# Kernel optimization log

Hardware: AMD Instinct MI355X
Metric: run time of the kernel (lower is better)

Reference implementation:

```python
import jax, jax.numpy as jnp
import numpy as np

GEOM_W = 0.01
N_ITERS = 3
HUBER_DELTA = 0.5
LM_EPS = 1e-6

def _skew(w):
    x, y, z = w[..., 0], w[..., 1], w[..., 2]
    o = jnp.zeros_like(x)
    return jnp.stack([jnp.stack([o, -z, y], -1),
                      jnp.stack([z, o, -x], -1),
                      jnp.stack([-y, x, o], -1)], -2)

def _se3_exp(xi):
    # xi = [omega(3), v(3)]; returns [B,4,4] left-multiplicative increment
    w, v = xi[:, :3], xi[:, 3:]
    th2 = jnp.sum(w * w, -1)
    small = th2 < 1e-8
    th2s = jnp.where(small, 1.0, th2)
    th = jnp.sqrt(th2s)
    A = jnp.where(small, 1.0 - th2 / 6.0, jnp.sin(th) / th)
    Bc = jnp.where(small, 0.5 - th2 / 24.0, (1.0 - jnp.cos(th)) / th2s)
    Cc = jnp.where(small, 1.0 / 6.0 - th2 / 120.0, (th - jnp.sin(th)) / (th2s * th))
    K = _skew(w)
    K2 = jnp.einsum('bij,bjk->bik', K, K)
    I3 = jnp.eye(3, dtype=xi.dtype)
    R = I3 + A[:, None, None] * K + Bc[:, None, None] * K2
    V = I3 + Bc[:, None, None] * K + Cc[:, None, None] * K2
    t = jnp.einsum('bij,bj->bi', V, v)
    T = jnp.zeros((xi.shape[0], 4, 4), xi.dtype)
    return T.at[:, :3, :3].set(R).at[:, :3, 3].set(t).at[:, 3, 3].set(1.0)

def _xy_grid(H, W, K):
    fx, fy, cx, cy = [K[:, i][:, None, None, None] for i in range(4)]
    uu = jnp.arange(W, dtype=K.dtype)[None, None, None, :]
    vv = jnp.arange(H, dtype=K.dtype)[None, None, :, None]
    return (uu - cx) / fx, (vv - cy) / fy  # [B,1,1,W], [B,1,H,1]

def _compute_vertex(d, px, py):
    return jnp.concatenate([px * d, py * d, d], 1)  # [B,3,H,W]

def _central_diff(F):
    fp = jnp.pad(F, ((0, 0), (0, 0), (0, 0), (1, 1)), mode='edge')
    dx = (fp[:, :, :, 2:] - fp[:, :, :, :-2]) * 0.5
    fp = jnp.pad(F, ((0, 0), (0, 0), (1, 1), (0, 0)), mode='edge')
    dy = (fp[:, :, 2:, :] - fp[:, :, :-2, :]) * 0.5
    return dx, dy

def _compute_normal(V):
    dvdx, dvdy = _central_diff(V)
    n = jnp.cross(jnp.moveaxis(dvdx, 1, -1), jnp.moveaxis(dvdy, 1, -1))
    n = jnp.moveaxis(n, -1, 1)
    return n / jnp.sqrt(jnp.sum(n * n, 1, keepdims=True) + 1e-12)

def _bilinear(F, u, v):
    # F [B,C,H,W]; u,v [B,N] pixel coords; zero padding bilinear -> [B,C,N]
    B, C, H, W = F.shape
    N = u.shape[1]
    u0, v0 = jnp.floor(u), jnp.floor(v)
    du, dv = u - u0, v - v0
    Ff = F.reshape(B, C, H * W)
    def gat(ui, vi, w):
        inb = (ui >= 0) & (ui <= W - 1) & (vi >= 0) & (vi <= H - 1)
        uc = jnp.clip(ui, 0, W - 1).astype(jnp.int32)
        vc = jnp.clip(vi, 0, H - 1).astype(jnp.int32)
        idx = jnp.broadcast_to((vc * W + uc)[:, None, :], (B, C, N))
        return jnp.take_along_axis(Ff, idx, axis=2) * (w * inb.astype(F.dtype))[:, None, :]
    return (gat(u0, v0, (1 - du) * (1 - dv)) + gat(u0 + 1, v0, du * (1 - dv)) +
            gat(u0, v0 + 1, (1 - du) * dv) + gat(u0 + 1, v0 + 1, du * dv))

def _grid_sample(F, grid):
    # grid [B,H,W,2] in [-1,1], align_corners=True, zero padding
    B, C, H, W = F.shape
    u = (grid[..., 0] + 1.0) * 0.5 * (W - 1)
    v = (grid[..., 1] + 1.0) * 0.5 * (H - 1)
    return _bilinear(F, u.reshape(B, -1), v.reshape(B, -1)).reshape(B, C, H, W)

def _icp_sigma(dpt, normal_r, R):
    sxy, sdisp, baseline, focal = 5.5, 0.4, 1.2, 525.0
    B, _, H, W = normal_r.shape
    sd = jnp.concatenate([dpt / focal * sxy, dpt / focal * sxy,
                          dpt * dpt * sdisp / (focal * baseline)], 1)
    J = jnp.einsum('bcn,bci->bin', normal_r.reshape(B, 3, H * W), R).reshape(B, 3, H, W)
    cov = jnp.sum(J * sd * sd * J, 1, keepdims=True)
    return jnp.sqrt(cov + 1e-8)

def _icp(V0, V1, N0, N1, T, K):
    B, _, H, W = V0.shape
    Np = H * W
    R, t = T[:, :3, :3], T[:, :3, 3]
    fx, fy, cx, cy = [K[:, i][:, None] for i in range(4)]
    V1f = V1.reshape(B, 3, Np)
    X = jnp.einsum('bij,bjn->bin', R, V1f) + t[:, :, None]
    x_, y_, s_ = X[:, 0], X[:, 1], X[:, 2]
    ss = jnp.where(jnp.abs(s_) > 1e-8, s_, 1e-8)
    u_ = x_ / ss * fx + cx
    v_ = y_ / ss * fy + cy
    inviews = (u_ > 0) & (u_ < W - 1) & (v_ > 0) & (v_ < H - 1)
    rV1 = _bilinear(V0, u_, v_)   # warp_features(vertex0)
    rN1 = _bilinear(N0, u_, v_)   # warp_features(normal0)
    diff = X - rV1
    dn = jnp.sqrt(jnp.sum(diff * diff, 1) + 1e-12)
    occ = (~inviews | (dn > 0.1)).reshape(B, 1, H, W)
    res = jnp.sum(rN1 * diff, 1).reshape(B, 1, H, W)
    NtC = jnp.einsum('bcn,bci->bni', rN1, R)              # [B,N,3]
    S = _skew(jnp.moveaxis(V1f, 1, -1))                   # [B,N,3,3]
    Jrot = jnp.einsum('bnj,bnjk->bnk', NtC, S)
    JFp = jnp.concatenate([Jrot, -NtC], -1)[:, None]      # [B,1,N,6]
    sigma = _icp_sigma(V1[:, 2:3], rN1.reshape(B, 3, H, W), R)
    res = res / (sigma + 1e-8)
    JFp = -JFp / (sigma.reshape(B, 1, Np, 1) + 1e-8)
    res = jnp.where(occ, 1e-6, res)
    return res, JFp, occ

def _forward(pose, I0, I1, invD0, invD1, intrinsics, depth0, depth1):
    B, C, H, W = I0.shape
    px, py = _xy_grid(H, W, intrinsics)
    fx, fy, cx, cy = [intrinsics[:, i][:, None, None] for i in range(4)]
    V0 = _compute_vertex(depth0, px, py)
    V1 = _compute_vertex(depth1, px, py)
    N0 = _compute_normal(V0)
    N1 = _compute_normal(V1)
    dI0x, dI0y = _central_diff(I0)  # feature_gradient (pose-independent, hoisted)
    eye3 = jnp.broadcast_to(jnp.eye(3, dtype=I0.dtype), (B, H, W, 3, 3))
    valid_depth = (depth0 > 0) & (depth1 > 0)
    for _ in range(N_ITERS):
        R, tt = pose[:, :3, :3], pose[:, :3, 3]
        X0 = jnp.einsum('bij,bjhw->bihw', R, V1) + tt[:, :, None, None]
        x, y, z = X0[:, 0], X0[:, 1], X0[:, 2]
        valid0 = z > 1e-8
        zs = jnp.where(jnp.abs(z) > 1e-8, z, 1e-8)
        u = fx * x / zs + cx
        v = fy * y / zs + cy
        zero = jnp.zeros_like(u)
        Jp = jnp.stack([jnp.stack([fx / zs, zero, -fx * x / (zs * zs)], -1),
                        jnp.stack([zero, fy / zs, -fy * y / (zs * zs)], -1)], -2)  # [B,H,W,2,3]
        Jt = jnp.concatenate([-_skew(jnp.moveaxis(X0, 1, -1)), eye3], -1)          # [B,H,W,3,6]
        Jw = jnp.einsum('bhwij,bhwjk->bhwik', Jp, Jt)                              # [B,H,W,2,6]
        inb = (u > 0) & (u < W - 1) & (v > 0) & (v < H - 1)
        valid = (inb & valid0)[:, None] & valid_depth                              # [B,1,H,W]
        grid = jnp.clip((jnp.stack([u / (W - 1), v / (H - 1)], -1) - 0.5) * 2.0, -2.0, 2.0)
        I0w = _grid_sample(I0, grid)
        r_I = I1 - I0w
        gI = jnp.stack([_grid_sample(dI0x, grid), _grid_sample(dI0y, grid)], -1)   # [B,C,H,W,2]
        J_I = jnp.einsum('bchwn,bhwnx->bchwx', gI, Jw)                             # [B,C,H,W,6]
        r_Z, J_Z, occ = _icp(V0, V1, N0, N1, pose, intrinsics)
        vflat = jnp.broadcast_to(valid, (B, C + 1, H, W)).reshape(B, -1).astype(I0.dtype)
        J = jnp.concatenate([J_I.reshape(B, -1, 6), GEOM_W * J_Z.reshape(B, -1, 6)], 1) * vflat[..., None]
        r = jnp.concatenate([r_I.reshape(B, -1), -GEOM_W * r_Z.reshape(B, -1)], 1) * vflat
        ar = jnp.abs(r)
        wts = jnp.where(ar <= HUBER_DELTA, 1.0, HUBER_DELTA / jnp.maximum(ar, 1e-12))  # Huber m-estimator
        JtJ = jnp.einsum('bni,bnj->bij', J, wts[..., None] * J)
        Hm = JtJ + LM_EPS * jnp.eye(6, dtype=J.dtype)                              # LM_H damping
        Rhs = jnp.einsum('bni,bn->bi', J, wts * r)
        xi = jnp.linalg.solve(Hm, Rhs[..., None])[..., 0]
        pose = jnp.einsum('bij,bjk->bik', _se3_exp(xi), pose)  # left-mult retr
    return pose

def setup_inputs() -> dict:
    key = jax.random.key(0)
    ks = jax.random.split(key, 6)
    B, C, H, W = 4, 8, 192, 256
    I0 = jax.random.normal(ks[0], (B, C, H, W), jnp.float32)
    I1 = jax.random.normal(ks[1], (B, C, H, W), jnp.float32)
    depth0 = jax.random.uniform(ks[2], (B, 1, H, W), jnp.float32, 0.5, 3.0)
    depth1 = jax.random.uniform(ks[3], (B, 1, H, W), jnp.float32, 0.5, 3.0)
    invD0, invD1 = 1.0 / depth0, 1.0 / depth1
    intrinsics = jnp.tile(jnp.array([[200.0, 200.0, 128.0, 96.0]], jnp.float32), (B, 1))
    pose = jnp.tile(jnp.eye(4, dtype=jnp.float32)[None], (B, 1, 1))
    pose = pose.at[:, :3, 3].set(0.01 * jax.random.normal(ks[4], (B, 3), jnp.float32))
    return dict(pose=pose, I0=I0, I1=I1, invD0=invD0, invD1=invD1,
                intrinsics=intrinsics, depth0=depth0, depth1=depth1)

def reference(pose, I0, I1, invD0, invD1, intrinsics, depth0, depth1):
    return _forward(pose, I0, I1, invD0, invD1, intrinsics, depth0, depth1)
```

## Files before the change

kernel.cpp:

```cpp
#include <hip/hip_runtime.h>
#include <math.h>

#define B_ 4
#define C_ 8
#define H_ 192
#define W_ 256
#define HW_ (H_*W_)
#define GEOMW 0.01f
#define HUBER 0.5f
#define LMEPS 1e-6f

#define N0_SZ  (B_*3*HW_)
#define ACC_SZ (3*B_*32)
#define POSE_SZ (B_*16)

typedef float f4a __attribute__((ext_vector_type(4), aligned(4)));
typedef float f2a __attribute__((ext_vector_type(2), aligned(4)));

__global__ void precompute_kernel(const float* __restrict__ depth0,
                                  const float* __restrict__ intr,
                                  const float* __restrict__ pose0,
                                  float* __restrict__ N0,
                                  float* __restrict__ acc,
                                  float* __restrict__ poseb) {
    int idx = blockIdx.x * blockDim.x + threadIdx.x;
    if (idx < ACC_SZ) acc[idx] = 0.f;
    if (idx < POSE_SZ) poseb[idx] = pose0[idx];
    if (idx >= B_ * HW_) return;
    int b = idx / HW_;
    int p = idx - b * HW_;
    int h = p >> 8;
    int w = p & 255;
    float fx = intr[b*4+0], fy = intr[b*4+1], cx = intr[b*4+2], cy = intr[b*4+3];
    const float* d = depth0 + b * HW_;
    int wl = max(w-1, 0), wr = min(w+1, W_-1);
    int hu = max(h-1, 0), hd = min(h+1, H_-1);
    float dr = d[h*W_ + wr], dl = d[h*W_ + wl];
    float dd = d[hd*W_ + w], du_ = d[hu*W_ + w];
    float pxr = ((float)wr - cx)/fx, pxl = ((float)wl - cx)/fx;
    float pyh = ((float)h  - cy)/fy;
    float pxw = ((float)w  - cx)/fx;
    float pyd = ((float)hd - cy)/fy, pyu = ((float)hu - cy)/fy;
    float dxx = 0.5f*(pxr*dr - pxl*dl), dxy = 0.5f*(pyh*dr - pyh*dl), dxz = 0.5f*(dr - dl);
    float dyx = 0.5f*(pxw*dd - pxw*du_), dyy = 0.5f*(pyd*dd - pyu*du_), dyz = 0.5f*(dd - du_);
    float n0 = dxy*dyz - dxz*dyy;
    float n1 = dxz*dyx - dxx*dyz;
    float n2 = dxx*dyy - dxy*dyx;
    float inv = 1.0f / sqrtf(n0*n0 + n1*n1 + n2*n2 + 1e-12f);
    N0[(b*3+0)*HW_ + p] = n0*inv;
    N0[(b*3+1)*HW_ + p] = n1*inv;
    N0[(b*3+2)*HW_ + p] = n2*inv;
}

__global__ __launch_bounds__(256)
void accumulate_kernel(const float* __restrict__ I0,
                       const float* __restrict__ I1,
                       const float* __restrict__ depth0,
                       const float* __restrict__ depth1,
                       const float* __restrict__ intr,
                       const float* __restrict__ N0,
                       const float* __restrict__ poseb,
                       float* __restrict__ acc) {
    const int b = blockIdx.y;
    const float* P = poseb + b*16;
    const float R00 = P[0],  R01 = P[1],  R02 = P[2],  t0 = P[3];
    const float R10 = P[4],  R11 = P[5],  R12 = P[6],  t1 = P[7];
    const float R20 = P[8],  R21 = P[9],  R22 = P[10], t2 = P[11];
    const float fx = intr[b*4+0], fy = intr[b*4+1], cx = intr[b*4+2], cy = intr[b*4+3];
    const float* I0b = I0 + b*C_*HW_;
    const float* I1b = I1 + b*C_*HW_;
    const float* d0b = depth0 + b*HW_;
    const float* d1b = depth1 + b*HW_;
    const float* N0b = N0 + b*3*HW_;
    float* accb = acc + b*32;

    float a[27];
#pragma unroll
    for (int i = 0; i < 27; i++) a[i] = 0.f;

#pragma unroll 2
    for (int item = 0; item < 6; ++item) {
        const int g = item*65536 + (int)blockIdx.x*256 + (int)threadIdx.x;
        const int c = g / HW_;
        const int p = g - c*HW_;
        const int h = p >> 8;
        const int w = p & 255;
        const float d1v = d1b[p];
        const float d0v = d0b[p];
        const float pxv = ((float)w - cx)/fx;
        const float pyv = ((float)h - cy)/fy;
        const float V1x = pxv*d1v, V1y = pyv*d1v, V1z = d1v;
        const float X = R00*V1x + R01*V1y + R02*V1z + t0;
        const float Y = R10*V1x + R11*V1y + R12*V1z + t1;
        const float Z = R20*V1x + R21*V1y + R22*V1z + t2;

        bool valid = (Z > 1e-8f) && (d0v > 0.f) && (d1v > 0.f);
        float u = 0.f, v = 0.f;
        if (valid) {
            u = fx*X/Z + cx;
            v = fy*Y/Z + cy;
            valid = (u > 0.f && u < (float)(W_-1) && v > 0.f && v < (float)(H_-1));
        }
        if (!valid) continue;

        const float u0f = floorf(u), v0f = floorf(v);
        const int u0 = (int)u0f, v0 = (int)v0f;
        const float du = u - u0f, dv = v - v0f;
        const float w00 = (1.f-du)*(1.f-dv), w10 = du*(1.f-dv);
        const float w01 = (1.f-du)*dv,       w11 = du*dv;
        const int i00 = v0*W_ + u0, i01 = i00 + W_;

        const float invz = 1.0f / Z;
        const float Jp00 = fx*invz, Jp02 = -fx*X*invz*invz;
        const float Jp11 = fy*invz, Jp12 = -fy*Y*invz*invz;
        float Jw0[6], Jw1[6];
        {
            const float Jt_[3][6] = {
                {0.f,  Z, -Y, 1.f, 0.f, 0.f},
                {-Z, 0.f,  X, 0.f, 1.f, 0.f},
                { Y,  -X, 0.f, 0.f, 0.f, 1.f}};
#pragma unroll
            for (int k = 0; k < 6; k++) {
                Jw0[k] = Jp00*Jt_[0][k] + Jp02*Jt_[2][k];
                Jw1[k] = Jp11*Jt_[1][k] + Jp12*Jt_[2][k];
            }
        }

        {
            const float* Ic = I0b + c*HW_;
            const int r0 = v0*W_, r1 = r0 + W_;
            const int rm = max(v0-1,0)*W_, rp = min(v0+2,H_-1)*W_;
            float fm0,f00,f10,fp0, fm1,f01,f11,fp1, g0a,g0b,g1a,g1b;
            if (u0 >= 1 && u0 <= W_-3) {
                const f4a A0 = *(const f4a*)(Ic + r0 + u0 - 1);
                const f4a A1 = *(const f4a*)(Ic + r1 + u0 - 1);
                const f2a Bm = *(const f2a*)(Ic + rm + u0);
                const f2a Bp = *(const f2a*)(Ic + rp + u0);
                fm0=A0.x; f00=A0.y; f10=A0.z; fp0=A0.w;
                fm1=A1.x; f01=A1.y; f11=A1.z; fp1=A1.w;
                g0a=Bm.x; g0b=Bm.y; g1a=Bp.x; g1b=Bp.y;
            } else {
                const int um = max(u0-1, 0), up = min(u0+2, W_-1);
                f00=Ic[r0+u0]; f10=Ic[r0+u0+1]; f01=Ic[r1+u0]; f11=Ic[r1+u0+1];
                fm0=Ic[r0+um]; fp0=Ic[r0+up];   fm1=Ic[r1+um]; fp1=Ic[r1+up];
                g0a=Ic[rm+u0]; g0b=Ic[rm+u0+1]; g1a=Ic[rp+u0]; g1b=Ic[rp+u0+1];
            }
            const float I0w = w00*f00 + w10*f10 + w01*f01 + w11*f11;
            const float gx00 = 0.5f*(f10 - fm0);
            const float gx10 = 0.5f*(fp0 - f00);
            const float gx01 = 0.5f*(f11 - fm1);
            const float gx11 = 0.5f*(fp1 - f01);
            const float gy00 = 0.5f*(f01 - g0a);
            const float gy10 = 0.5f*(f11 - g0b);
            const float gy01 = 0.5f*(g1a - f00);
            const float gy11 = 0.5f*(g1b - f10);
            const float gx = w00*gx00 + w10*gx10 + w01*gx01 + w11*gx11;
            const float gy = w00*gy00 + w10*gy10 + w01*gy01 + w11*gy11;
            const float rv = I1b[c*HW_ + p] - I0w;
            float Jr[6];
#pragma unroll
            for (int k = 0; k < 6; k++) Jr[k] = gx*Jw0[k] + gy*Jw1[k];
            const float ar = fabsf(rv);
            const float wt = (ar <= HUBER) ? 1.f : HUBER / fmaxf(ar, 1e-12f);
            int cnt = 0;
#pragma unroll
            for (int i2 = 0; i2 < 6; i2++) {
                const float wJ = wt * Jr[i2];
#pragma unroll
                for (int j2 = i2; j2 < 6; j2++) a[cnt++] += wJ * Jr[j2];
                a[21+i2] += wJ * rv;
            }
        }

        if (c == 0) {
            const f2a D0 = *(const f2a*)(d0b + i00);
            const f2a D1 = *(const f2a*)(d0b + i01);
            const float dc00 = D0.x, dc10 = D0.y, dc01 = D1.x, dc11 = D1.y;
            const float pxu0 = ((float)u0 - cx)/fx, pxu1 = ((float)(u0+1) - cx)/fx;
            const float pyv0 = ((float)v0 - cy)/fy, pyv1 = ((float)(v0+1) - cy)/fy;
            const float rVx = w00*pxu0*dc00 + w10*pxu1*dc10 + w01*pxu0*dc01 + w11*pxu1*dc11;
            const float rVy = w00*pyv0*dc00 + w10*pyv0*dc10 + w01*pyv1*dc01 + w11*pyv1*dc11;
            const float rVz = w00*dc00 + w10*dc10 + w01*dc01 + w11*dc11;
            float rN[3];
#pragma unroll
            for (int cc = 0; cc < 3; cc++) {
                const float* Nc = N0b + cc*HW_;
                const f2a Na = *(const f2a*)(Nc + i00);
                const f2a Nb = *(const f2a*)(Nc + i01);
                rN[cc] = w00*Na.x + w10*Na.y + w01*Nb.x + w11*Nb.y;
            }
            const float dfx = X - rVx, dfy = Y - rVy, dfz = Z - rVz;
            const float dn = sqrtf(dfx*dfx + dfy*dfy + dfz*dfz + 1e-12f);
            const bool occ = dn > 0.1f;
            const float res = rN[0]*dfx + rN[1]*dfy + rN[2]*dfz;
            const float NtC0 = rN[0]*R00 + rN[1]*R10 + rN[2]*R20;
            const float NtC1 = rN[0]*R01 + rN[1]*R11 + rN[2]*R21;
            const float NtC2 = rN[0]*R02 + rN[1]*R12 + rN[2]*R22;
            const float Jr0 = NtC1*V1z - NtC2*V1y;
            const float Jr1 = NtC2*V1x - NtC0*V1z;
            const float Jr2 = NtC0*V1y - NtC1*V1x;
            const float sd0 = d1v * (5.5f/525.0f);
            const float sd2 = d1v * d1v * (0.4f/(525.0f*1.2f));
            const float cov = (NtC0*NtC0 + NtC1*NtC1)*sd0*sd0 + NtC2*NtC2*sd2*sd2;
            const float sigma = sqrtf(cov + 1e-8f);
            const float invs = 1.0f/(sigma + 1e-8f);
            const float rZ = occ ? 1e-6f : res*invs;
            float Jr[6];
            Jr[0] = GEOMW * (-Jr0*invs);
            Jr[1] = GEOMW * (-Jr1*invs);
            Jr[2] = GEOMW * (-Jr2*invs);
            Jr[3] = GEOMW * ( NtC0*invs);
            Jr[4] = GEOMW * ( NtC1*invs);
            Jr[5] = GEOMW * ( NtC2*invs);
            const float rv = -GEOMW * rZ;
            const float ar = fabsf(rv);
            const float wt = (ar <= HUBER) ? 1.f : HUBER / fmaxf(ar, 1e-12f);
            int cnt = 0;
#pragma unroll
            for (int i2 = 0; i2 < 6; i2++) {
                const float wJ = wt * Jr[i2];
#pragma unroll
                for (int j2 = i2; j2 < 6; j2++) a[cnt++] += wJ * Jr[j2];
                a[21+i2] += wJ * rv;
            }
        }
    }

    __shared__ float red[4][27];
    const int wid  = threadIdx.x >> 6;
    const int lane = threadIdx.x & 63;
#pragma unroll
    for (int k = 0; k < 27; k++) {
        float val = a[k];
        for (int off = 32; off > 0; off >>= 1)
            val += __shfl_down(val, off, 64);
        if (lane == 0) red[wid][k] = val;
    }
    __syncthreads();
    if (threadIdx.x < 27) {
        const int k = threadIdx.x;
        atomicAdd(&accb[k], red[0][k] + red[1][k] + red[2][k] + red[3][k]);
    }
}

__global__ void solve_kernel(const float* __restrict__ acc,
                             float* __restrict__ poseb,
                             float* __restrict__ out) {
    int b = threadIdx.x;
    if (b >= B_) return;
    const float* a = acc + b*32;
    float M[6][7];
    {
        int cnt = 0;
        float Hm[6][6];
        for (int i = 0; i < 6; i++)
            for (int j = i; j < 6; j++) { Hm[i][j] = a[cnt]; Hm[j][i] = a[cnt]; cnt++; }
        for (int i = 0; i < 6; i++) {
            for (int j = 0; j < 6; j++) M[i][j] = Hm[i][j];
            M[i][i] += LMEPS;
            M[i][6] = a[21+i];
        }
    }
    for (int k = 0; k < 6; k++) {
        int piv = k; float mx = fabsf(M[k][k]);
        for (int r = k+1; r < 6; r++) { float vv = fabsf(M[r][k]); if (vv > mx) { mx = vv; piv = r; } }
        if (piv != k)
            for (int j = 0; j < 7; j++) { float tmp = M[k][j]; M[k][j] = M[piv][j]; M[piv][j] = tmp; }
        const float inv = 1.0f / M[k][k];
        for (int r = k+1; r < 6; r++) {
            const float f = M[r][k] * inv;
            for (int j = k; j < 7; j++) M[r][j] -= f * M[k][j];
        }
    }
    float xi[6];
    for (int i = 5; i >= 0; i--) {
        float s = M[i][6];
        for (int j = i+1; j < 6; j++) s -= M[i][j]*xi[j];
        xi[i] = s / M[i][i];
    }
    const float wx = xi[0], wy = xi[1], wz = xi[2];
    const float th2 = wx*wx + wy*wy + wz*wz;
    float A, Bc, Cc;
    if (th2 < 1e-8f) {
        A  = 1.f - th2/6.f;
        Bc = 0.5f - th2/24.f;
        Cc = 1.f/6.f - th2/120.f;
    } else {
        const float th = sqrtf(th2);
        const float s = sinf(th), cth = cosf(th);
        A  = s/th;
        Bc = (1.f - cth)/th2;
        Cc = (th - s)/(th2*th);
    }
    float K[3][3] = {{0.f, -wz, wy}, {wz, 0.f, -wx}, {-wy, wx, 0.f}};
    float K2[3][3];
    for (int i = 0; i < 3; i++)
        for (int j = 0; j < 3; j++)
            K2[i][j] = K[i][0]*K[0][j] + K[i][1]*K[1][j] + K[i][2]*K[2][j];
    float Re[3][3], Vm[3][3];
    for (int i = 0; i < 3; i++)
        for (int j = 0; j < 3; j++) {
            const float eye = (i == j) ? 1.f : 0.f;
            Re[i][j] = eye + A*K[i][j] + Bc*K2[i][j];
            Vm[i][j] = eye + Bc*K[i][j] + Cc*K2[i][j];
        }
    float tt[3];
    for (int i = 0; i < 3; i++)
        tt[i] = Vm[i][0]*xi[3] + Vm[i][1]*xi[4] + Vm[i][2]*xi[5];
    float Pold[16], Pnew[16];
    for (int i = 0; i < 16; i++) Pold[i] = poseb[b*16 + i];
    for (int j = 0; j < 4; j++) {
        for (int i = 0; i < 3; i++)
            Pnew[i*4+j] = Re[i][0]*Pold[0*4+j] + Re[i][1]*Pold[1*4+j] + Re[i][2]*Pold[2*4+j] + tt[i]*Pold[3*4+j];
        Pnew[3*4+j] = Pold[3*4+j];
    }
    for (int i = 0; i < 16; i++) { poseb[b*16 + i] = Pnew[i]; out[b*16 + i] = Pnew[i]; }
}

extern "C" void kernel_launch(void* const* d_in, const int* in_sizes, int n_in,
                              void* d_out, int out_size, void* d_ws, size_t ws_size,
                              hipStream_t stream) {
    const float* pose0  = (const float*)d_in[0];
    const float* I0     = (const float*)d_in[1];
    const float* I1     = (const float*)d_in[2];
    const float* intr   = (const float*)d_in[5];
    const float* depth0 = (const float*)d_in[6];
    const float* depth1 = (const float*)d_in[7];
    float* ws    = (float*)d_ws;
    float* N0    = ws;
    float* acc   = ws + N0_SZ;
    float* poseb = acc + ACC_SZ;
    float* out   = (float*)d_out;

    precompute_kernel<<<(B_*HW_ + 255)/256, 256, 0, stream>>>(depth0, intr, pose0, N0, acc, poseb);
    for (int it = 0; it < 3; it++) {
        accumulate_kernel<<<dim3(256, B_), 256, 0, stream>>>(
            I0, I1, depth0, depth1, intr, N0, poseb, acc + it*B_*32);
        solve_kernel<<<1, 64, 0, stream>>>(acc + it*B_*32, poseb, out);
    }
}
```

Baseline: 167.7 us.

## Make accumulate loop branch-free, double grid, add occupancy bound and reciprocal intrinsics

Replaces the early `continue` for invalid projections with clamped coordinates and a validity mask folded into the Huber weight, so every lane runs the same gather path without divergence. Doubles the grid to 512 blocks per batch, halves the per-thread loop to 3 fully unrolled items, and adds a min-blocks hint of 5 to `__launch_bounds__` to favour occupancy. Divisions by fx/fy are replaced with multiplies by precomputed reciprocals. The cost is that invalid pixels now do redundant loads and arithmetic, and the tighter register cap could force spills given the 27 accumulators.

```diff
diff --git a/kernel.cpp b/kernel.cpp
--- a/kernel.cpp
+++ b/kernel.cpp
@@ -52,7 +52,7 @@
     N0[(b*3+2)*HW_ + p] = n2*inv;
 }
 
-__global__ __launch_bounds__(256)
+__global__ __launch_bounds__(256, 5)
 void accumulate_kernel(const float* __restrict__ I0,
                        const float* __restrict__ I1,
                        const float* __restrict__ depth0,
@@ -67,6 +67,7 @@
     const float R10 = P[4],  R11 = P[5],  R12 = P[6],  t1 = P[7];
     const float R20 = P[8],  R21 = P[9],  R22 = P[10], t2 = P[11];
     const float fx = intr[b*4+0], fy = intr[b*4+1], cx = intr[b*4+2], cy = intr[b*4+3];
+    const float ifx = 1.0f/fx, ify = 1.0f/fy;
     const float* I0b = I0 + b*C_*HW_;
     const float* I1b = I1 + b*C_*HW_;
     const float* d0b = depth0 + b*HW_;
@@ -78,30 +79,33 @@
 #pragma unroll
     for (int i = 0; i < 27; i++) a[i] = 0.f;
 
-#pragma unroll 2
-    for (int item = 0; item < 6; ++item) {
-        const int g = item*65536 + (int)blockIdx.x*256 + (int)threadIdx.x;
+#pragma unroll
+    for (int item = 0; item < 3; ++item) {
+        const int g = item*131072 + (int)blockIdx.x*256 + (int)threadIdx.x;
         const int c = g / HW_;
         const int p = g - c*HW_;
         const int h = p >> 8;
         const int w = p & 255;
         const float d1v = d1b[p];
         const float d0v = d0b[p];
-        const float pxv = ((float)w - cx)/fx;
-        const float pyv = ((float)h - cy)/fy;
+        const float pxv = ((float)w - cx)*ifx;
+        const float pyv = ((float)h - cy)*ify;
         const float V1x = pxv*d1v, V1y = pyv*d1v, V1z = d1v;
-        const float X = R00*V1x + R01*V1y + R02*V1z + t0;
-        const float Y = R10*V1x + R11*V1y + R12*V1z + t1;
-        const float Z = R20*V1x + R21*V1y + R22*V1z + t2;
-
-        bool valid = (Z > 1e-8f) && (d0v > 0.f) && (d1v > 0.f);
-        float u = 0.f, v = 0.f;
-        if (valid) {
-            u = fx*X/Z + cx;
-            v = fy*Y/Z + cy;
-            valid = (u > 0.f && u < (float)(W_-1) && v > 0.f && v < (float)(H_-1));
-        }
-        if (!valid) continue;
+        const float X0 = R00*V1x + R01*V1y + R02*V1z + t0;
+        const float Y0 = R10*V1x + R11*V1y + R12*V1z + t1;
+        const float Z0 = R20*V1x + R21*V1y + R22*V1z + t2;
+
+        bool valid = (Z0 > 1e-8f) && (d0v > 0.f) && (d1v > 0.f);
+        const float Z = valid ? Z0 : 1.0f;
+        const float X = valid ? X0 : 0.0f;
+        const float Y = valid ? Y0 : 0.0f;
+        const float invz = 1.0f / Z;
+        float u = fx*X*invz + cx;
+        float v = fy*Y*invz + cy;
+        valid = valid && (u > 0.f && u < (float)(W_-1) && v > 0.f && v < (float)(H_-1));
+        u = valid ? u : 1.5f;
+        v = valid ? v : 1.5f;
+        const float vm = valid ? 1.f : 0.f;
 
         const float u0f = floorf(u), v0f = floorf(v);
         const int u0 = (int)u0f, v0 = (int)v0f;
@@ -110,7 +114,6 @@
         const float w01 = (1.f-du)*dv,       w11 = du*dv;
         const int i00 = v0*W_ + u0, i01 = i00 + W_;
 
-        const float invz = 1.0f / Z;
         const float Jp00 = fx*invz, Jp02 = -fx*X*invz*invz;
         const float Jp11 = fy*invz, Jp12 = -fy*Y*invz*invz;
         float Jw0[6], Jw1[6];
@@ -161,7 +164,7 @@
 #pragma unroll
             for (int k = 0; k < 6; k++) Jr[k] = gx*Jw0[k] + gy*Jw1[k];
             const float ar = fabsf(rv);
-            const float wt = (ar <= HUBER) ? 1.f : HUBER / fmaxf(ar, 1e-12f);
+            const float wt = vm * ((ar <= HUBER) ? 1.f : HUBER / fmaxf(ar, 1e-12f));
             int cnt = 0;
 #pragma unroll
             for (int i2 = 0; i2 < 6; i2++) {
@@ -176,8 +179,8 @@
             const f2a D0 = *(const f2a*)(d0b + i00);
             const f2a D1 = *(const f2a*)(d0b + i01);
             const float dc00 = D0.x, dc10 = D0.y, dc01 = D1.x, dc11 = D1.y;
-            const float pxu0 = ((float)u0 - cx)/fx, pxu1 = ((float)(u0+1) - cx)/fx;
-            const float pyv0 = ((float)v0 - cy)/fy, pyv1 = ((float)(v0+1) - cy)/fy;
+            const float pxu0 = ((float)u0 - cx)*ifx, pxu1 = ((float)(u0+1) - cx)*ifx;
+            const float pyv0 = ((float)v0 - cy)*ify, pyv1 = ((float)(v0+1) - cy)*ify;
             const float rVx = w00*pxu0*dc00 + w10*pxu1*dc10 + w01*pxu0*dc01 + w11*pxu1*dc11;
             const float rVy = w00*pyv0*dc00 + w10*pyv0*dc10 + w01*pyv1*dc01 + w11*pyv1*dc11;
             const float rVz = w00*dc00 + w10*dc10 + w01*dc01 + w11*dc11;
@@ -214,7 +217,7 @@
             Jr[5] = GEOMW * ( NtC2*invs);
             const float rv = -GEOMW * rZ;
             const float ar = fabsf(rv);
-            const float wt = (ar <= HUBER) ? 1.f : HUBER / fmaxf(ar, 1e-12f);
+            const float wt = vm * ((ar <= HUBER) ? 1.f : HUBER / fmaxf(ar, 1e-12f));
             int cnt = 0;
 #pragma unroll
             for (int i2 = 0; i2 < 6; i2++) {
@@ -334,7 +337,7 @@
 
     precompute_kernel<<<(B_*HW_ + 255)/256, 256, 0, stream>>>(depth0, intr, pose0, N0, acc, poseb);
     for (int it = 0; it < 3; it++) {
-        accumulate_kernel<<<dim3(256, B_), 256, 0, stream>>>(
+        accumulate_kernel<<<dim3(512, B_), 256, 0, stream>>>(
             I0, I1, depth0, depth1, intr, N0, poseb, acc + it*B_*32);
         solve_kernel<<<1, 64, 0, stream>>>(acc + it*B_*32, poseb, out);
     }
```

Result: slower. 237.2 us (+41.4%).
